# Kernel tuning notes

Hardware: AMD Instinct MI355X
Metric: run time of the kernel (lower is better)

The kernel has to match this reference:

```python
import jax, jax.numpy as jnp
import numpy as np

N = 50000      # nodes
E = 800000     # edges (before self-loops)
H = 8          # attention heads
C = 16         # hidden per head (n_hid)
CH = H * C     # 128 = concat channel width
L = 3          # n_layer
F_IN = 128     # n_feat
N_CLASS = 40
NEG_SLOPE = 0.2


def setup_inputs() -> dict:
    key = jax.random.key(0)
    ks = jax.random.split(key, 14)
    s = 0.1
    return {
        "x": jax.random.normal(ks[0], (N, F_IN), jnp.float32),
        "edge_index": jax.random.randint(ks[1], (2, E), 0, N, jnp.int32),
        # layer 0: in F_IN -> H heads of C
        "W0":   jax.random.normal(ks[2], (F_IN, H * C), jnp.float32) * s,
        "as0":  jax.random.normal(ks[3], (H, C), jnp.float32) * s,
        "ad0":  jax.random.normal(ks[4], (H, C), jnp.float32) * s,
        "b0":   jnp.zeros((H * C,), jnp.float32),
        # layers 1..L-1 (stacked): in CH -> H heads of C
        "W12":  jax.random.normal(ks[5], (L - 1, CH, H * C), jnp.float32) * s,
        "as12": jax.random.normal(ks[6], (L - 1, H, C), jnp.float32) * s,
        "ad12": jax.random.normal(ks[7], (L - 1, H, C), jnp.float32) * s,
        "b12":  jnp.zeros((L - 1, H * C), jnp.float32),
        # attention-based skip aggregation over layers
        "Watt": jax.random.normal(ks[8], (CH, CH), jnp.float32) * s,
        "aatt": jax.random.normal(ks[9], (CH,), jnp.float32) * s,
        # output head
        "Wout": jax.random.normal(ks[10], (CH, N_CLASS), jnp.float32) * s,
        "bout": jnp.zeros((N_CLASS,), jnp.float32),
    }


def _gat_layer(x, W, a_src, a_dst, b, src, dst):
    # x: [N, F]; W: [F, H*C]; a_src/a_dst: [H, C]; b: [H*C]
    h = (x @ W).reshape(N, H, C)                                 # [N,H,C]
    s_src = jnp.einsum("nhc,hc->nh", h, a_src)                   # [N,H]
    s_dst = jnp.einsum("nhc,hc->nh", h, a_dst)                   # [N,H]
    e = jax.nn.leaky_relu(s_src[src] + s_dst[dst], NEG_SLOPE)    # [Et,H]
    # segment softmax over incoming edges of each dst node
    e_max = jax.ops.segment_max(e, dst, num_segments=N)          # [N,H]
    ee = jnp.exp(e - e_max[dst])
    denom = jax.ops.segment_sum(ee, dst, num_segments=N)         # [N,H]
    alpha = ee / (denom[dst] + 1e-16)                            # [Et,H]
    msg = h[src] * alpha[:, :, None]                             # [Et,H,C]
    out = jax.ops.segment_sum(msg, dst, num_segments=N)          # [N,H,C]
    return out.reshape(N, H * C) + b


def reference(x, edge_index, W0, as0, ad0, b0, W12, as12, ad12, b12,
              Watt, aatt, Wout, bout):
    src, dst = edge_index[0], edge_index[1]
    loops = jnp.arange(N, dtype=src.dtype)                       # self-loops (PyG default)
    src = jnp.concatenate([src, loops])
    dst = jnp.concatenate([dst, loops])

    h = jax.nn.elu(_gat_layer(x, W0, as0, ad0, b0, src, dst))
    hs = [h]
    for l in range(L - 1):
        h = jax.nn.elu(_gat_layer(h, W12[l], as12[l], ad12[l], b12[l], src, dst))
        hs.append(h)

    hstack = jnp.stack(hs, axis=1)                               # [N,L,CH]
    scores = jnp.einsum("nlc,c->nl", jnp.tanh(jnp.einsum("nlc,cd->nld", hstack, Watt)), aatt)
    lam = jax.nn.softmax(scores, axis=1)                         # [N,L] over layers
    hfinal = jnp.einsum("nlc,nl->nc", hstack, lam)               # [N,CH]
    return hfinal @ Wout + bout
```

## Files before the change

kernel.cpp:

```cpp
#include <hip/hip_runtime.h>
#include <hip/hip_bf16.h>

typedef float f32x4 __attribute__((ext_vector_type(4)));
typedef short bf16x8 __attribute__((ext_vector_type(8)));

#define BCAP 20480

__device__ __forceinline__ float4 ld4(const float* p){ return *reinterpret_cast<const float4*>(p); }
__device__ __forceinline__ unsigned short f2bf(float f){
  unsigned int u = __float_as_uint(f);
  u = (u + 0x7fffu + ((u>>16)&1u)) >> 16;
  return (unsigned short)u;
}
__device__ __forceinline__ float bflo(unsigned int u){ return __uint_as_float(u<<16); }
__device__ __forceinline__ float bfhi(unsigned int u){ return __uint_as_float(u & 0xffff0000u); }
__device__ __forceinline__ float bfs(short s){ return __uint_as_float(((unsigned)(unsigned short)s)<<16); }
__device__ __forceinline__ float ftanh(float x){
  float e = __expf(2.f*x);
  return fmaf(-2.f, __builtin_amdgcn_rcpf(e+1.f), 1.f);
}

__global__ __launch_bounds__(256) void k_prep_bucket(
    const float* __restrict__ W0, const float* __restrict__ W12, const float* __restrict__ Watt,
    const float* __restrict__ as0, const float* __restrict__ ad0,
    const float* __restrict__ as12, const float* __restrict__ ad12,
    const float* __restrict__ Wout, unsigned short* __restrict__ dst,
    const int* __restrict__ ei, int* __restrict__ bcnt, unsigned* __restrict__ bdata,
    int E_, int Et)
{
  __shared__ char smraw[32768];
  int b = blockIdx.x, t = threadIdx.x;
  if (b < 5){
    if (b == 4){
      unsigned short* wo = dst + (size_t)4*18432;
      for (int i=t; i<48*128; i+=256){
        int col = i>>7, k = i&127;
        float v = (col < 40) ? Wout[(size_t)k*40 + col] : 0.f;
        unsigned short hi = f2bf(v);
        float r = v - __uint_as_float(((unsigned)hi)<<16);
        wo[i] = hi;
        wo[48*128 + i] = f2bf(r);
      }
      return;
    }
    float* Wf = (float*)smraw;
    const float* W = (b==0) ? W0 : (b==3 ? Watt : W12 + (size_t)(b-1)*16384);
    unsigned short* out = dst + (size_t)b*18432;
    const float* as_ = (b==0) ? as0 : as12 + (size_t)(b-1)*128;
    const float* ad_ = (b==0) ? ad0 : ad12 + (size_t)(b-1)*128;

    for (int half=0; half<2; half++){
      #pragma unroll
      for (int p=0;p<8;p++){
        int i = p*256 + t;
        *reinterpret_cast<float4*>(&Wf[i*4]) = ld4(&W[(size_t)half*8192 + i*4]);
      }
      __syncthreads();
      {
        int col = t>>1, koff = (t&1)*32;
        #pragma unroll
        for (int j=0;j<4;j++){
          unsigned short tmp[8];
          #pragma unroll
          for (int q=0;q<8;q++) tmp[q] = f2bf(Wf[(koff + j*8 + q)*128 + col]);
          *reinterpret_cast<uint4*>(&out[col*128 + half*64 + koff + j*8]) = *reinterpret_cast<const uint4*>(tmp);
        }
      }
      {
        int ce = t>>4;
        int h  = ce & 7;
        if (b < 3){
          const float* av = (ce < 8) ? (as_ + h*16) : (ad_ + h*16);
          float avr[16];
          #pragma unroll
          for (int c2=0;c2<16;c2++) avr[c2] = av[c2];
          #pragma unroll
          for (int i=0;i<4;i++){
            int kl = (t&15) + i*16;
            float s = 0.f;
            #pragma unroll
            for (int c2=0;c2<16;c2++) s += Wf[kl*128 + h*16 + c2]*avr[c2];
            out[(128+ce)*128 + half*64 + kl] = f2bf(s);
          }
        } else {
          #pragma unroll
          for (int i=0;i<4;i++){
            int kl = (t&15) + i*16;
            out[(128+ce)*128 + half*64 + kl] = 0;
          }
        }
      }
      __syncthreads();
    }
    return;
  }
  int* h    = (int*)smraw;
  int* base = (int*)(smraw + 256);
  if (t < 64) h[t] = 0;
  __syncthreads();
  int e0 = (b-5)*2048 + t;
  int dv[8], sv[8], rv[8];
  #pragma unroll
  for (int k=0;k<8;k++){
    int e = e0 + k*256;
    if (e < Et){
      int s, d;
      if (e < E_){ s = ei[e]; d = ei[E_+e]; } else { s = e-E_; d = s; }
      dv[k] = d; sv[k] = s;
      rv[k] = atomicAdd(&h[d>>10], 1);
    } else dv[k] = -1;
  }
  __syncthreads();
  if (t < 64 && h[t]) base[t] = atomicAdd(&bcnt[t], h[t]);
  __syncthreads();
  #pragma unroll
  for (int k=0;k<8;k++){
    if (dv[k] >= 0){
      int bk = dv[k]>>10;
      bdata[(size_t)bk*BCAP + base[bk] + rv[k]] = ((unsigned)(dv[k]&1023)<<17) | (unsigned)sv[k];
    }
  }
}

__global__ __launch_bounds__(512) void k_bfinish_gemm0(
    const unsigned* __restrict__ bdata, const int* __restrict__ bcnt,
    int* __restrict__ off, int* __restrict__ csr, int N_, int nb,
    const float* __restrict__ x, const unsigned short* __restrict__ Bt,
    unsigned short* __restrict__ C, float* __restrict__ s_src, float* __restrict__ s_dst)
{
  __shared__ int c[1024];
  __shared__ int wsum[8];
  __shared__ int bbase_s;
  int t = threadIdx.x;
  if ((int)blockIdx.x < nb){
    int b = blockIdx.x;
    if (t < 64){
      int v = (t < nb) ? bcnt[t] : 0;
      int incl = v;
      #pragma unroll
      for (int d=1; d<64; d<<=1){ int u = __shfl_up(incl, d); if (t>=d) incl += u; }
      if (t == b) bbase_s = incl - v;
      if (b == 0 && t == 63) off[N_] = incl;
    }
    int cnt = bcnt[b];
    size_t lo = (size_t)b*BCAP;
    for (int i=t;i<1024;i+=512) c[i]=0;
    __syncthreads();
    for (int i=t; i<cnt; i+=512) atomicAdd(&c[bdata[lo+i]>>17], 1);
    __syncthreads();
    int c0 = c[2*t], c1 = c[2*t+1];
    int s = c0 + c1;
    int lane = t&63, w = t>>6;
    int incl = s;
    #pragma unroll
    for (int d=1; d<64; d<<=1){ int u = __shfl_up(incl, d); if (lane>=d) incl += u; }
    if (lane==63) wsum[w] = incl;
    __syncthreads();
    int wpre = 0;
    #pragma unroll
    for (int k=0;k<8;k++) if (k<w) wpre += wsum[k];
    int run = bbase_s + wpre + incl - s;
    int n = (b<<10) + 2*t;
    if (n   < N_) off[n]   = run;
    if (n+1 < N_) off[n+1] = run + c0;
    c[2*t]   = run;
    c[2*t+1] = run + c0;
    __syncthreads();
    for (int i=t; i<cnt; i+=512){
      unsigned p = bdata[lo+i];
      int pos = atomicAdd(&c[p>>17], 1);
      csr[pos] = (int)(p & 0x1FFFFu);
    }
    return;
  }
  if (t >= 256) return;
  int lane = t & 63, w = t >> 6;
  int rA = lane & 15, g = lane >> 4;
  int r0 = (blockIdx.x - nb)*128 + w*32;
  f32x4 z = {0.f,0.f,0.f,0.f};
  f32x4 acc[2][9];
  #pragma unroll
  for (int mf=0;mf<2;mf++)
    #pragma unroll
    for (int nf=0;nf<9;nf++) acc[mf][nf] = z;

  int M = N_;
  int rowc0 = min(r0 + rA,      M-1);
  int rowc1 = min(r0 + 16 + rA, M-1);
  #pragma unroll
  for (int ks=0; ks<4; ks++){
    int ko = ks*32 + g*8;
    bf16x8 a0, a1;
    float4 v0 = ld4(&x[(size_t)rowc0*128 + ko]);
    float4 v1 = ld4(&x[(size_t)rowc0*128 + ko + 4]);
    float4 v2 = ld4(&x[(size_t)rowc1*128 + ko]);
    float4 v3 = ld4(&x[(size_t)rowc1*128 + ko + 4]);
    a0[0]=(short)f2bf(v0.x); a0[1]=(short)f2bf(v0.y); a0[2]=(short)f2bf(v0.z); a0[3]=(short)f2bf(v0.w);
    a0[4]=(short)f2bf(v1.x); a0[5]=(short)f2bf(v1.y); a0[6]=(short)f2bf(v1.z); a0[7]=(short)f2bf(v1.w);
    a1[0]=(short)f2bf(v2.x); a1[1]=(short)f2bf(v2.y); a1[2]=(short)f2bf(v2.z); a1[3]=(short)f2bf(v2.w);
    a1[4]=(short)f2bf(v3.x); a1[5]=(short)f2bf(v3.y); a1[6]=(short)f2bf(v3.z); a1[7]=(short)f2bf(v3.w);
    #pragma unroll
    for (int nf=0;nf<9;nf++){
      bf16x8 bf_ = *reinterpret_cast<const bf16x8*>(Bt + (size_t)(nf*16+rA)*128 + ko);
      acc[0][nf] = __builtin_amdgcn_mfma_f32_16x16x32_bf16(a0, bf_, acc[0][nf], 0, 0, 0);
      acc[1][nf] = __builtin_amdgcn_mfma_f32_16x16x32_bf16(a1, bf_, acc[1][nf], 0, 0, 0);
    }
  }

  #pragma unroll
  for (int mf=0;mf<2;mf++){
    #pragma unroll
    for (int r=0;r<4;r++){
      int row = r0 + mf*16 + g*4 + r;
      if (row < M){
        #pragma unroll
        for (int nf=0;nf<8;nf++) C[(size_t)row*128 + nf*16 + rA] = f2bf(acc[mf][nf][r]);
        float sv_ = acc[mf][8][r];
        if (rA < 8) s_src[(size_t)row*8 + rA]     = sv_;
        else        s_dst[(size_t)row*8 + rA - 8] = sv_;
      }
    }
  }
}

__global__ __launch_bounds__(256) void k_gemm(
    const unsigned short* __restrict__ A, const unsigned short* __restrict__ Bt,
    unsigned short* __restrict__ C, float* __restrict__ s_src, float* __restrict__ s_dst, int M)
{
  int t = threadIdx.x, lane = t & 63, w = t >> 6;
  int rA = lane & 15, g = lane >> 4;
  int r0 = blockIdx.x*128 + w*32;
  f32x4 z = {0.f,0.f,0.f,0.f};
  f32x4 acc[2][9];
  #pragma unroll
  for (int mf=0;mf<2;mf++)
    #pragma unroll
    for (int nf=0;nf<9;nf++) acc[mf][nf] = z;

  int rowc0 = min(r0 + rA,      M-1);
  int rowc1 = min(r0 + 16 + rA, M-1);
  #pragma unroll
  for (int ks=0; ks<4; ks++){
    int ko = ks*32 + g*8;
    bf16x8 a0 = *reinterpret_cast<const bf16x8*>(A + (size_t)rowc0*128 + ko);
    bf16x8 a1 = *reinterpret_cast<const bf16x8*>(A + (size_t)rowc1*128 + ko);
    #pragma unroll
    for (int nf=0;nf<9;nf++){
      bf16x8 bf_ = *reinterpret_cast<const bf16x8*>(Bt + (size_t)(nf*16+rA)*128 + ko);
      acc[0][nf] = __builtin_amdgcn_mfma_f32_16x16x32_bf16(a0, bf_, acc[0][nf], 0, 0, 0);
      acc[1][nf] = __builtin_amdgcn_mfma_f32_16x16x32_bf16(a1, bf_, acc[1][nf], 0, 0, 0);
    }
  }

  #pragma unroll
  for (int mf=0;mf<2;mf++){
    #pragma unroll
    for (int r=0;r<4;r++){
      int row = r0 + mf*16 + g*4 + r;
      if (row < M){
        #pragma unroll
        for (int nf=0;nf<8;nf++) C[(size_t)row*128 + nf*16 + rA] = f2bf(acc[mf][nf][r]);
        float sv_ = acc[mf][8][r];
        if (rA < 8) s_src[(size_t)row*8 + rA]     = sv_;
        else        s_dst[(size_t)row*8 + rA - 8] = sv_;
      }
    }
  }
}

__global__ __launch_bounds__(256) void k_aggregate(
    const int* __restrict__ off, const int* __restrict__ csr,
    const unsigned short* __restrict__ htmp, const float* __restrict__ s_src,
    const float* __restrict__ s_dst, const float* __restrict__ bias,
    unsigned short* __restrict__ hout, int N_)
{
  __shared__ float esc[4][2][288];
  __shared__ int   ssrc[4][2][32];
  int w = threadIdx.x >> 6;
  int lane = threadIdx.x & 63;
  int half = lane >> 5;
  int l32  = lane & 31;
  int c2   = l32 & 15;
  int eo   = l32 >> 4;
  int myh  = c2 >> 1;
  int n = blockIdx.x*8 + w*2 + half;
  int base = 0, deg = 0;
  if (n < N_){ base = off[n]; deg = off[n+1] - base; }
  float sdv[8] = {0.f,0.f,0.f,0.f,0.f,0.f,0.f,0.f};
  if (n < N_){
    float4 sd0 = ld4(&s_dst[(size_t)n*8]);
    float4 sd1 = ld4(&s_dst[(size_t)n*8+4]);
    sdv[0]=sd0.x; sdv[1]=sd0.y; sdv[2]=sd0.z; sdv[3]=sd0.w;
    sdv[4]=sd1.x; sdv[5]=sd1.y; sdv[6]=sd1.z; sdv[7]=sd1.w;
  }
  float acc0=0.f,acc1=0.f,acc2=0.f,acc3=0.f,acc4=0.f,acc5=0.f,acc6=0.f,acc7=0.f;
  float dsum = 0.f;
  const char* hb = (const char*)htmp + (c2<<4);

  for (int cb=0; cb<deg; cb+=32){
    int cdeg = min(32, deg-cb);
    int srcj = 0;
    float ee[8];
    if (l32 < cdeg){
      srcj = csr[base+cb+l32];
      float4 a0 = ld4(&s_src[(size_t)srcj*8]);
      float4 a1 = ld4(&s_src[(size_t)srcj*8+4]);
      float sv[8] = {a0.x,a0.y,a0.z,a0.w,a1.x,a1.y,a1.z,a1.w};
      #pragma unroll
      for (int h=0;h<8;h++){
        float v = sv[h] + sdv[h];
        v = v > 0.f ? v : 0.2f*v;
        ee[h] = __expf(v);
      }
    } else {
      #pragma unroll
      for (int h=0;h<8;h++) ee[h] = 0.f;
    }
    ssrc[w][half][l32] = srcj;
    #pragma unroll
    for (int h=0;h<8;h++) esc[w][half][h*36 + l32] = ee[h];
    asm volatile("s_waitcnt lgkmcnt(0)" ::: "memory");
    __builtin_amdgcn_sched_barrier(0);

    for (int j=0; j<cdeg; j+=4){
      int e0 = j + eo;
      int e1 = j + 2 + eo;
      int s0 = ssrc[w][half][e0];
      int s1 = ssrc[w][half][e1];
      float ev0 = esc[w][half][myh*36 + e0];
      float ev1 = esc[w][half][myh*36 + e1];
      uint4 u0 = *reinterpret_cast<const uint4*>(hb + ((size_t)(unsigned)s0<<8));
      uint4 u1 = *reinterpret_cast<const uint4*>(hb + ((size_t)(unsigned)s1<<8));
      acc0 = fmaf(ev0, bflo(u0.x), acc0);
      acc1 = fmaf(ev0, bfhi(u0.x), acc1);
      acc2 = fmaf(ev0, bflo(u0.y), acc2);
      acc3 = fmaf(ev0, bfhi(u0.y), acc3);
      acc4 = fmaf(ev0, bflo(u0.z), acc4);
      acc5 = fmaf(ev0, bfhi(u0.z), acc5);
      acc6 = fmaf(ev0, bflo(u0.w), acc6);
      acc7 = fmaf(ev0, bfhi(u0.w), acc7);
      acc0 = fmaf(ev1, bflo(u1.x), acc0);
      acc1 = fmaf(ev1, bfhi(u1.x), acc1);
      acc2 = fmaf(ev1, bflo(u1.y), acc2);
      acc3 = fmaf(ev1, bfhi(u1.y), acc3);
      acc4 = fmaf(ev1, bflo(u1.z), acc4);
      acc5 = fmaf(ev1, bfhi(u1.z), acc5);
      acc6 = fmaf(ev1, bflo(u1.w), acc6);
      acc7 = fmaf(ev1, bfhi(u1.w), acc7);
      dsum += ev0 + ev1;
    }
  }
  acc0 += __shfl_xor(acc0, 16);
  acc1 += __shfl_xor(acc1, 16);
  acc2 += __shfl_xor(acc2, 16);
  acc3 += __shfl_xor(acc3, 16);
  acc4 += __shfl_xor(acc4, 16);
  acc5 += __shfl_xor(acc5, 16);
  acc6 += __shfl_xor(acc6, 16);
  acc7 += __shfl_xor(acc7, 16);
  dsum += __shfl_xor(dsum, 16);

  if (n < N_ && eo == 0){
    float inv = 1.f/(dsum + 1e-16f);
    float4 b0 = ld4(&bias[c2*8]);
    float4 b1 = ld4(&bias[c2*8+4]);
    float o0 = fmaf(acc0, inv, b0.x);
    float o1 = fmaf(acc1, inv, b0.y);
    float o2 = fmaf(acc2, inv, b0.z);
    float o3 = fmaf(acc3, inv, b0.w);
    float o4 = fmaf(acc4, inv, b1.x);
    float o5 = fmaf(acc5, inv, b1.y);
    float o6 = fmaf(acc6, inv, b1.z);
    float o7 = fmaf(acc7, inv, b1.w);
    o0 = o0>0.f ? o0 : (__expf(o0)-1.f);
    o1 = o1>0.f ? o1 : (__expf(o1)-1.f);
    o2 = o2>0.f ? o2 : (__expf(o2)-1.f);
    o3 = o3>0.f ? o3 : (__expf(o3)-1.f);
    o4 = o4>0.f ? o4 : (__expf(o4)-1.f);
    o5 = o5>0.f ? o5 : (__expf(o5)-1.f);
    o6 = o6>0.f ? o6 : (__expf(o6)-1.f);
    o7 = o7>0.f ? o7 : (__expf(o7)-1.f);
    uint4 pk;
    pk.x = (unsigned)f2bf(o0) | ((unsigned)f2bf(o1)<<16);
    pk.y = (unsigned)f2bf(o2) | ((unsigned)f2bf(o3)<<16);
    pk.z = (unsigned)f2bf(o4) | ((unsigned)f2bf(o5)<<16);
    pk.w = (unsigned)f2bf(o6) | ((unsigned)f2bf(o7)<<16);
    *reinterpret_cast<uint4*>(&hout[(size_t)n*128 + c2*8]) = pk;
  }
}

__global__ __launch_bounds__(256) void k_final4(
    const unsigned short* __restrict__ h0, const unsigned short* __restrict__ h1,
    const unsigned short* __restrict__ h2,
    const unsigned short* __restrict__ WattT, const float* __restrict__ aatt,
    const unsigned short* __restrict__ WoutT,
    const float* __restrict__ bout, float* __restrict__ out, int M)
{
  int t = threadIdx.x, lane = t & 63, w = t >> 6;
  int rA = lane & 15, g = lane >> 4;
  int r0 = blockIdx.x*64 + w*16;
  int rowc = min(r0 + rA, M-1);

  float av[8];
  #pragma unroll
  for (int nf=0;nf<8;nf++) av[nf] = aatt[nf*16 + rA];

  bf16x8 a[3][4];
  #pragma unroll
  for (int ks=0;ks<4;ks++){
    int ko = ks*32 + g*8;
    a[0][ks] = *reinterpret_cast<const bf16x8*>(h0 + (size_t)rowc*128 + ko);
    a[1][ks] = *reinterpret_cast<const bf16x8*>(h1 + (size_t)rowc*128 + ko);
    a[2][ks] = *reinterpret_cast<const bf16x8*>(h2 + (size_t)rowc*128 + ko);
  }

  float sc[3][4];
  #pragma unroll
  for (int l=0;l<3;l++)
    #pragma unroll
    for (int r=0;r<4;r++) sc[l][r] = 0.f;

  #pragma unroll
  for (int ch=0; ch<4; ch++){
    f32x4 acc[3][2];
    #pragma unroll
    for (int l=0;l<3;l++){ acc[l][0] = (f32x4){0.f,0.f,0.f,0.f}; acc[l][1] = (f32x4){0.f,0.f,0.f,0.f}; }
    #pragma unroll
    for (int ks=0; ks<4; ks++){
      int ko = ks*32 + g*8;
      bf16x8 b0 = *reinterpret_cast<const bf16x8*>(WattT + (size_t)((ch*2+0)*16+rA)*128 + ko);
      bf16x8 b1 = *reinterpret_cast<const bf16x8*>(WattT + (size_t)((ch*2+1)*16+rA)*128 + ko);
      #pragma unroll
      for (int l=0;l<3;l++){
        acc[l][0] = __builtin_amdgcn_mfma_f32_16x16x32_bf16(a[l][ks], b0, acc[l][0], 0, 0, 0);
        acc[l][1] = __builtin_amdgcn_mfma_f32_16x16x32_bf16(a[l][ks], b1, acc[l][1], 0, 0, 0);
      }
    }
    float w0 = av[ch*2], w1 = av[ch*2+1];
    #pragma unroll
    for (int l=0;l<3;l++)
      #pragma unroll
      for (int r=0;r<4;r++)
        sc[l][r] += ftanh(acc[l][0][r])*w0 + ftanh(acc[l][1][r])*w1;
  }
  #pragma unroll
  for (int l=0;l<3;l++)
    #pragma unroll
    for (int r=0;r<4;r++){
      float s = sc[l][r];
      s += __shfl_xor(s, 1);
      s += __shfl_xor(s, 2);
      s += __shfl_xor(s, 4);
      s += __shfl_xor(s, 8);
      sc[l][r] = s;
    }

  float lam[3][4];
  #pragma unroll
  for (int r=0;r<4;r++){
    float m = fmaxf(sc[0][r], fmaxf(sc[1][r], sc[2][r]));
    float e0 = __expf(sc[0][r]-m), e1 = __expf(sc[1][r]-m), e2 = __expf(sc[2][r]-m);
    float inv = 1.f/(e0+e1+e2);
    lam[0][r]=e0*inv; lam[1][r]=e1*inv; lam[2][r]=e2*inv;
  }
  int rsel = rA & 3;
  int srcLane = ((rA>>2)<<4) | rA;
  float p0 = rsel==0 ? lam[0][0] : rsel==1 ? lam[0][1] : rsel==2 ? lam[0][2] : lam[0][3];
  float p1 = rsel==0 ? lam[1][0] : rsel==1 ? lam[1][1] : rsel==2 ? lam[1][2] : lam[1][3];
  float p2 = rsel==0 ? lam[2][0] : rsel==1 ? lam[2][1] : rsel==2 ? lam[2][2] : lam[2][3];
  float lamA[3];
  lamA[0] = __shfl(p0, srcLane);
  lamA[1] = __shfl(p1, srcLane);
  lamA[2] = __shfl(p2, srcLane);

  f32x4 oacc[3];
  #pragma unroll
  for (int nf=0;nf<3;nf++) oacc[nf] = (f32x4){0.f,0.f,0.f,0.f};
  #pragma unroll
  for (int ks=0;ks<4;ks++){
    int ko = ks*32 + g*8;
    bf16x8 asc[3];
    #pragma unroll
    for (int l=0;l<3;l++){
      #pragma unroll
      for (int i=0;i<8;i++) asc[l][i] = (short)f2bf(bfs(a[l][ks][i]) * lamA[l]);
    }
    #pragma unroll
    for (int nf=0;nf<3;nf++){
      bf16x8 bh = *reinterpret_cast<const bf16x8*>(WoutT + (size_t)(nf*16+rA)*128 + ko);
      bf16x8 bl = *reinterpret_cast<const bf16x8*>(WoutT + 6144 + (size_t)(nf*16+rA)*128 + ko);
      #pragma unroll
      for (int l=0;l<3;l++){
        oacc[nf] = __builtin_amdgcn_mfma_f32_16x16x32_bf16(asc[l], bh, oacc[nf], 0, 0, 0);
        oacc[nf] = __builtin_amdgcn_mfma_f32_16x16x32_bf16(asc[l], bl, oacc[nf], 0, 0, 0);
      }
    }
  }

  #pragma unroll
  for (int nf=0;nf<3;nf++){
    int col = nf*16 + rA;
    float bv = (col < 40) ? bout[col] : 0.f;
    #pragma unroll
    for (int r=0;r<4;r++){
      int row = r0 + g*4 + r;
      if (row < M && col < 40) out[(size_t)row*40 + col] = oacc[nf][r] + bv;
    }
  }
}

extern "C" void kernel_launch(void* const* d_in, const int* in_sizes, int n_in,
                              void* d_out, int out_size, void* d_ws, size_t ws_size,
                              hipStream_t stream)
{
  const float* x    = (const float*)d_in[0];
  const int*   ei   = (const int*)d_in[1];
  const float* W0   = (const float*)d_in[2];
  const float* as0  = (const float*)d_in[3];
  const float* ad0  = (const float*)d_in[4];
  const float* b0   = (const float*)d_in[5];
  const float* W12  = (const float*)d_in[6];
  const float* as12 = (const float*)d_in[7];
  const float* ad12 = (const float*)d_in[8];
  const float* b12  = (const float*)d_in[9];
  const float* Watt = (const float*)d_in[10];
  const float* aatt = (const float*)d_in[11];
  const float* Wout = (const float*)d_in[12];
  const float* bout = (const float*)d_in[13];
  const int N_ = in_sizes[0] / 128;
  const int E_ = in_sizes[1] / 2;
  const int Et = E_ + N_;
  const int nb = (N_ + 1023) >> 10;

  char* p = (char*)d_ws;
  auto carve = [&](size_t bytes)->char*{ char* r = p; p += (bytes + 255) & ~(size_t)255; return r; };
  unsigned short* htmp = (unsigned short*)carve((size_t)N_*128*2);
  unsigned short* h0   = (unsigned short*)carve((size_t)N_*128*2);
  unsigned short* h1   = (unsigned short*)carve((size_t)N_*128*2);
  unsigned short* h2   = (unsigned short*)carve((size_t)N_*128*2);
  unsigned short* wsT  = (unsigned short*)carve((size_t)(5*18432 + 48*128)*2);
  float* ssrc_s  = (float*)carve((size_t)N_*8*4);
  float* sdst_s  = (float*)carve((size_t)N_*8*4);
  int* offv      = (int*)carve((size_t)(N_+1)*4);
  int* bcnt      = (int*)carve((size_t)64*4);
  unsigned* bdata= (unsigned*)carve((size_t)64*BCAP*4);
  int* csr       = (int*)carve((size_t)(Et+8)*4);

  hipMemsetAsync(bcnt, 0, 64*4, stream);
  int gB = (Et + 2047)/2048;
  int gM = (N_+127)/128;
  k_prep_bucket<<<5+gB,256,0,stream>>>(W0, W12, Watt, as0, ad0, as12, ad12, Wout, wsT,
                                       ei, bcnt, bdata, E_, Et);
  k_bfinish_gemm0<<<nb+gM,512,0,stream>>>(bdata, bcnt, offv, csr, N_, nb,
                                          x, wsT, htmp, ssrc_s, sdst_s);

  int gN8 = (N_+7)/8;
  int gF  = (N_+63)/64;
  unsigned short* hl[3] = {h0,h1,h2};
  for (int l=0;l<3;l++){
    const float* bb = (l==0)? b0 : b12 + (size_t)(l-1)*128;
    if (l > 0)
      k_gemm<<<gM,256,0,stream>>>(hl[l-1], wsT + (size_t)l*18432, htmp, ssrc_s, sdst_s, N_);
    k_aggregate<<<gN8,256,0,stream>>>(offv, csr, htmp, ssrc_s, sdst_s, bb, hl[l], N_);
  }
  k_final4<<<gF,256,0,stream>>>(h0, h1, h2, wsT + (size_t)3*18432, aatt,
                                wsT + (size_t)4*18432, bout, (float*)d_out, N_);
}
```

Baseline: 235.0 us.

## Split aggregation channels across two blocks per node group

The GAT aggregation kernel now launches twice as many blocks. Each block handles half of the 128 channels (4 of the 8 heads) for its 8 destination nodes, and within a half-wave each 8-lane group covers 8 edges instead of 16 lanes covering 2 edges. This raises parallelism and halves the softmax score work and LDS per block. In exchange, the CSR indices and source scores are reloaded by both halves, and each gathered row is read in 128-byte halves, giving less contiguous gathers and an extra shuffle-reduction stage.

```diff
diff --git a/kernel.cpp b/kernel.cpp
--- a/kernel.cpp
+++ b/kernel.cpp
@@ -274,61 +274,61 @@
     const float* __restrict__ s_dst, const float* __restrict__ bias,
     unsigned short* __restrict__ hout, int N_)
 {
-  __shared__ float esc[4][2][288];
+  __shared__ float esc[4][2][144];
   __shared__ int   ssrc[4][2][32];
-  int w = threadIdx.x >> 6;
-  int lane = threadIdx.x & 63;
+  int t = threadIdx.x;
+  int w = t >> 6;
+  int lane = t & 63;
   int half = lane >> 5;
   int l32  = lane & 31;
-  int c2   = l32 & 15;
-  int eo   = l32 >> 4;
-  int myh  = c2 >> 1;
-  int n = blockIdx.x*8 + w*2 + half;
+  int c8   = l32 & 7;
+  int eo   = l32 >> 3;
+  int hl   = c8 >> 1;
+  int p    = blockIdx.x & 1;
+  int ng   = blockIdx.x >> 1;
+  int n = ng*8 + w*2 + half;
   int base = 0, deg = 0;
   if (n < N_){ base = off[n]; deg = off[n+1] - base; }
-  float sdv[8] = {0.f,0.f,0.f,0.f,0.f,0.f,0.f,0.f};
+  float sdv[4] = {0.f,0.f,0.f,0.f};
   if (n < N_){
-    float4 sd0 = ld4(&s_dst[(size_t)n*8]);
-    float4 sd1 = ld4(&s_dst[(size_t)n*8+4]);
-    sdv[0]=sd0.x; sdv[1]=sd0.y; sdv[2]=sd0.z; sdv[3]=sd0.w;
-    sdv[4]=sd1.x; sdv[5]=sd1.y; sdv[6]=sd1.z; sdv[7]=sd1.w;
+    float4 sd = ld4(&s_dst[(size_t)n*8 + p*4]);
+    sdv[0]=sd.x; sdv[1]=sd.y; sdv[2]=sd.z; sdv[3]=sd.w;
   }
   float acc0=0.f,acc1=0.f,acc2=0.f,acc3=0.f,acc4=0.f,acc5=0.f,acc6=0.f,acc7=0.f;
   float dsum = 0.f;
-  const char* hb = (const char*)htmp + (c2<<4);
+  const char* hb = (const char*)htmp + (p<<7) + (c8<<4);
 
   for (int cb=0; cb<deg; cb+=32){
     int cdeg = min(32, deg-cb);
     int srcj = 0;
-    float ee[8];
+    float ee[4];
     if (l32 < cdeg){
       srcj = csr[base+cb+l32];
-      float4 a0 = ld4(&s_src[(size_t)srcj*8]);
-      float4 a1 = ld4(&s_src[(size_t)srcj*8+4]);
-      float sv[8] = {a0.x,a0.y,a0.z,a0.w,a1.x,a1.y,a1.z,a1.w};
-      #pragma unroll
-      for (int h=0;h<8;h++){
+      float4 a0 = ld4(&s_src[(size_t)srcj*8 + p*4]);
+      float sv[4] = {a0.x,a0.y,a0.z,a0.w};
+      #pragma unroll
+      for (int h=0;h<4;h++){
         float v = sv[h] + sdv[h];
         v = v > 0.f ? v : 0.2f*v;
         ee[h] = __expf(v);
       }
     } else {
       #pragma unroll
-      for (int h=0;h<8;h++) ee[h] = 0.f;
+      for (int h=0;h<4;h++) ee[h] = 0.f;
     }
     ssrc[w][half][l32] = srcj;
     #pragma unroll
-    for (int h=0;h<8;h++) esc[w][half][h*36 + l32] = ee[h];
+    for (int h=0;h<4;h++) esc[w][half][h*36 + l32] = ee[h];
     asm volatile("s_waitcnt lgkmcnt(0)" ::: "memory");
     __builtin_amdgcn_sched_barrier(0);
 
-    for (int j=0; j<cdeg; j+=4){
+    for (int j=0; j<cdeg; j+=8){
       int e0 = j + eo;
-      int e1 = j + 2 + eo;
+      int e1 = j + 4 + eo;
       int s0 = ssrc[w][half][e0];
       int s1 = ssrc[w][half][e1];
-      float ev0 = esc[w][half][myh*36 + e0];
-      float ev1 = esc[w][half][myh*36 + e1];
+      float ev0 = esc[w][half][hl*36 + e0];
+      float ev1 = esc[w][half][hl*36 + e1];
       uint4 u0 = *reinterpret_cast<const uint4*>(hb + ((size_t)(unsigned)s0<<8));
       uint4 u1 = *reinterpret_cast<const uint4*>(hb + ((size_t)(unsigned)s1<<8));
       acc0 = fmaf(ev0, bflo(u0.x), acc0);
@@ -350,20 +350,21 @@
       dsum += ev0 + ev1;
     }
   }
-  acc0 += __shfl_xor(acc0, 16);
-  acc1 += __shfl_xor(acc1, 16);
-  acc2 += __shfl_xor(acc2, 16);
-  acc3 += __shfl_xor(acc3, 16);
-  acc4 += __shfl_xor(acc4, 16);
-  acc5 += __shfl_xor(acc5, 16);
-  acc6 += __shfl_xor(acc6, 16);
-  acc7 += __shfl_xor(acc7, 16);
-  dsum += __shfl_xor(dsum, 16);
+  acc0 += __shfl_xor(acc0, 8);  acc0 += __shfl_xor(acc0, 16);
+  acc1 += __shfl_xor(acc1, 8);  acc1 += __shfl_xor(acc1, 16);
+  acc2 += __shfl_xor(acc2, 8);  acc2 += __shfl_xor(acc2, 16);
+  acc3 += __shfl_xor(acc3, 8);  acc3 += __shfl_xor(acc3, 16);
+  acc4 += __shfl_xor(acc4, 8);  acc4 += __shfl_xor(acc4, 16);
+  acc5 += __shfl_xor(acc5, 8);  acc5 += __shfl_xor(acc5, 16);
+  acc6 += __shfl_xor(acc6, 8);  acc6 += __shfl_xor(acc6, 16);
+  acc7 += __shfl_xor(acc7, 8);  acc7 += __shfl_xor(acc7, 16);
+  dsum += __shfl_xor(dsum, 8);  dsum += __shfl_xor(dsum, 16);
 
   if (n < N_ && eo == 0){
     float inv = 1.f/(dsum + 1e-16f);
-    float4 b0 = ld4(&bias[c2*8]);
-    float4 b1 = ld4(&bias[c2*8+4]);
+    int cbase = p*64 + c8*8;
+    float4 b0 = ld4(&bias[cbase]);
+    float4 b1 = ld4(&bias[cbase+4]);
     float o0 = fmaf(acc0, inv, b0.x);
     float o1 = fmaf(acc1, inv, b0.y);
     float o2 = fmaf(acc2, inv, b0.z);
@@ -385,7 +386,7 @@
     pk.y = (unsigned)f2bf(o2) | ((unsigned)f2bf(o3)<<16);
     pk.z = (unsigned)f2bf(o4) | ((unsigned)f2bf(o5)<<16);
     pk.w = (unsigned)f2bf(o6) | ((unsigned)f2bf(o7)<<16);
-    *reinterpret_cast<uint4*>(&hout[(size_t)n*128 + c2*8]) = pk;
+    *reinterpret_cast<uint4*>(&hout[(size_t)n*128 + cbase]) = pk;
   }
 }
 
@@ -554,14 +555,14 @@
   k_bfinish_gemm0<<<nb+gM,512,0,stream>>>(bdata, bcnt, offv, csr, N_, nb,
                                           x, wsT, htmp, ssrc_s, sdst_s);
 
-  int gN8 = (N_+7)/8;
+  int gA  = ((N_+7)/8)*2;
   int gF  = (N_+63)/64;
   unsigned short* hl[3] = {h0,h1,h2};
   for (int l=0;l<3;l++){
     const float* bb = (l==0)? b0 : b12 + (size_t)(l-1)*128;
     if (l > 0)
       k_gemm<<<gM,256,0,stream>>>(hl[l-1], wsT + (size_t)l*18432, htmp, ssrc_s, sdst_s, N_);
-    k_aggregate<<<gN8,256,0,stream>>>(offv, csr, htmp, ssrc_s, sdst_s, bb, hl[l], N_);
+    k_aggregate<<<gA,256,0,stream>>>(offv, csr, htmp, ssrc_s, sdst_s, bb, hl[l], N_);
   }
   k_final4<<<gF,256,0,stream>>>(h0, h1, h2, wsT + (size_t)3*18432, aatt,
                                 wsT + (size_t)4*18432, bout, (float*)d_out, N_);
```

After: 238.1 us. About the same (+1.3%).

## Fuse next-layer GEMM into aggregation epilogue with ping-pong buffers

Applied to the files above, without the earlier changes.

Removes the standalone GEMM kernel. After each aggregation block writes its 8 output rows, it also stages them in shared memory and runs the next layer's projection (features plus attention scores) with MFMA. Double-buffered htmp and score arrays keep reads of the current layer's projection separate from writes of the next layer's. This saves two launches and a global re-read of the hidden state. In exchange, each 8-row block reloads the full weight matrix, only half of each MFMA tile holds useful rows, and only two of the four waves do the GEMM work.

```diff
diff --git a/kernel.cpp b/kernel.cpp
--- a/kernel.cpp
+++ b/kernel.cpp
@@ -223,59 +223,18 @@
   }
 }
 
-__global__ __launch_bounds__(256) void k_gemm(
-    const unsigned short* __restrict__ A, const unsigned short* __restrict__ Bt,
-    unsigned short* __restrict__ C, float* __restrict__ s_src, float* __restrict__ s_dst, int M)
-{
-  int t = threadIdx.x, lane = t & 63, w = t >> 6;
-  int rA = lane & 15, g = lane >> 4;
-  int r0 = blockIdx.x*128 + w*32;
-  f32x4 z = {0.f,0.f,0.f,0.f};
-  f32x4 acc[2][9];
-  #pragma unroll
-  for (int mf=0;mf<2;mf++)
-    #pragma unroll
-    for (int nf=0;nf<9;nf++) acc[mf][nf] = z;
-
-  int rowc0 = min(r0 + rA,      M-1);
-  int rowc1 = min(r0 + 16 + rA, M-1);
-  #pragma unroll
-  for (int ks=0; ks<4; ks++){
-    int ko = ks*32 + g*8;
-    bf16x8 a0 = *reinterpret_cast<const bf16x8*>(A + (size_t)rowc0*128 + ko);
-    bf16x8 a1 = *reinterpret_cast<const bf16x8*>(A + (size_t)rowc1*128 + ko);
-    #pragma unroll
-    for (int nf=0;nf<9;nf++){
-      bf16x8 bf_ = *reinterpret_cast<const bf16x8*>(Bt + (size_t)(nf*16+rA)*128 + ko);
-      acc[0][nf] = __builtin_amdgcn_mfma_f32_16x16x32_bf16(a0, bf_, acc[0][nf], 0, 0, 0);
-      acc[1][nf] = __builtin_amdgcn_mfma_f32_16x16x32_bf16(a1, bf_, acc[1][nf], 0, 0, 0);
-    }
-  }
-
-  #pragma unroll
-  for (int mf=0;mf<2;mf++){
-    #pragma unroll
-    for (int r=0;r<4;r++){
-      int row = r0 + mf*16 + g*4 + r;
-      if (row < M){
-        #pragma unroll
-        for (int nf=0;nf<8;nf++) C[(size_t)row*128 + nf*16 + rA] = f2bf(acc[mf][nf][r]);
-        float sv_ = acc[mf][8][r];
-        if (rA < 8) s_src[(size_t)row*8 + rA]     = sv_;
-        else        s_dst[(size_t)row*8 + rA - 8] = sv_;
-      }
-    }
-  }
-}
-
-__global__ __launch_bounds__(256) void k_aggregate(
+template<int FUSE>
+__global__ __launch_bounds__(256) void k_agg_gemm(
     const int* __restrict__ off, const int* __restrict__ csr,
     const unsigned short* __restrict__ htmp, const float* __restrict__ s_src,
     const float* __restrict__ s_dst, const float* __restrict__ bias,
-    unsigned short* __restrict__ hout, int N_)
+    unsigned short* __restrict__ hout, int N_,
+    const unsigned short* __restrict__ Btn,
+    unsigned short* __restrict__ Cn, float* __restrict__ s_srcn, float* __restrict__ s_dstn)
 {
   __shared__ float esc[4][2][288];
   __shared__ int   ssrc[4][2][32];
+  __shared__ unsigned short hrows[8][128];
   int w = threadIdx.x >> 6;
   int lane = threadIdx.x & 63;
   int half = lane >> 5;
@@ -386,6 +345,45 @@
     pk.z = (unsigned)f2bf(o4) | ((unsigned)f2bf(o5)<<16);
     pk.w = (unsigned)f2bf(o6) | ((unsigned)f2bf(o7)<<16);
     *reinterpret_cast<uint4*>(&hout[(size_t)n*128 + c2*8]) = pk;
+    if (FUSE)
+      *reinterpret_cast<uint4*>(&hrows[w*2+half][c2*8]) = pk;
+  }
+
+  if (FUSE){
+    __syncthreads();
+    if (w < 2){
+      int rA2 = lane & 15, g2 = lane >> 4;
+      int rr = rA2 & 7;
+      bf16x8 a2[4];
+      #pragma unroll
+      for (int ks=0;ks<4;ks++)
+        a2[ks] = *reinterpret_cast<const bf16x8*>(&hrows[rr][ks*32 + g2*8]);
+      int n0 = blockIdx.x*8;
+      int nfLo = (w==0) ? 0 : 5;
+      int nfHi = (w==0) ? 5 : 9;
+      for (int nf=nfLo; nf<nfHi; nf++){
+        f32x4 acc2 = {0.f,0.f,0.f,0.f};
+        #pragma unroll
+        for (int ks=0;ks<4;ks++){
+          bf16x8 bf_ = *reinterpret_cast<const bf16x8*>(Btn + (size_t)(nf*16+rA2)*128 + ks*32 + g2*8);
+          acc2 = __builtin_amdgcn_mfma_f32_16x16x32_bf16(a2[ks], bf_, acc2, 0, 0, 0);
+        }
+        if (g2 < 2){
+          #pragma unroll
+          for (int r=0;r<4;r++){
+            int row = g2*4 + r;
+            int n2 = n0 + row;
+            if (n2 < N_){
+              if (nf < 8) Cn[(size_t)n2*128 + nf*16 + rA2] = f2bf(acc2[r]);
+              else {
+                if (rA2 < 8) s_srcn[(size_t)n2*8 + rA2]     = acc2[r];
+                else         s_dstn[(size_t)n2*8 + rA2 - 8] = acc2[r];
+              }
+            }
+          }
+        }
+      }
+    }
   }
 }
 
@@ -534,13 +532,16 @@
 
   char* p = (char*)d_ws;
   auto carve = [&](size_t bytes)->char*{ char* r = p; p += (bytes + 255) & ~(size_t)255; return r; };
-  unsigned short* htmp = (unsigned short*)carve((size_t)N_*128*2);
+  unsigned short* htmpA = (unsigned short*)carve((size_t)N_*128*2);
+  unsigned short* htmpB = (unsigned short*)carve((size_t)N_*128*2);
   unsigned short* h0   = (unsigned short*)carve((size_t)N_*128*2);
   unsigned short* h1   = (unsigned short*)carve((size_t)N_*128*2);
   unsigned short* h2   = (unsigned short*)carve((size_t)N_*128*2);
   unsigned short* wsT  = (unsigned short*)carve((size_t)(5*18432 + 48*128)*2);
-  float* ssrc_s  = (float*)carve((size_t)N_*8*4);
-  float* sdst_s  = (float*)carve((size_t)N_*8*4);
+  float* ssrcA  = (float*)carve((size_t)N_*8*4);
+  float* sdstA  = (float*)carve((size_t)N_*8*4);
+  float* ssrcB  = (float*)carve((size_t)N_*8*4);
+  float* sdstB  = (float*)carve((size_t)N_*8*4);
   int* offv      = (int*)carve((size_t)(N_+1)*4);
   int* bcnt      = (int*)carve((size_t)64*4);
   unsigned* bdata= (unsigned*)carve((size_t)64*BCAP*4);
@@ -552,17 +553,16 @@
   k_prep_bucket<<<5+gB,256,0,stream>>>(W0, W12, Watt, as0, ad0, as12, ad12, Wout, wsT,
                                        ei, bcnt, bdata, E_, Et);
   k_bfinish_gemm0<<<nb+gM,512,0,stream>>>(bdata, bcnt, offv, csr, N_, nb,
-                                          x, wsT, htmp, ssrc_s, sdst_s);
+                                          x, wsT, htmpA, ssrcA, sdstA);
 
   int gN8 = (N_+7)/8;
   int gF  = (N_+63)/64;
-  unsigned short* hl[3] = {h0,h1,h2};
-  for (int l=0;l<3;l++){
-    const float* bb = (l==0)? b0 : b12 + (size_t)(l-1)*128;
-    if (l > 0)
-      k_gemm<<<gM,256,0,stream>>>(hl[l-1], wsT + (size_t)l*18432, htmp, ssrc_s, sdst_s, N_);
-    k_aggregate<<<gN8,256,0,stream>>>(offv, csr, htmp, ssrc_s, sdst_s, bb, hl[l], N_);
-  }
+  k_agg_gemm<1><<<gN8,256,0,stream>>>(offv, csr, htmpA, ssrcA, sdstA, b0, h0, N_,
+                                      wsT + (size_t)1*18432, htmpB, ssrcB, sdstB);
+  k_agg_gemm<1><<<gN8,256,0,stream>>>(offv, csr, htmpB, ssrcB, sdstB, b12, h1, N_,
+                                      wsT + (size_t)2*18432, htmpA, ssrcA, sdstA);
+  k_agg_gemm<0><<<gN8,256,0,stream>>>(offv, csr, htmpA, ssrcA, sdstA, b12 + 128, h2, N_,
+                                      nullptr, nullptr, nullptr, nullptr);
   k_final4<<<gF,256,0,stream>>>(h0, h1, h2, wsT + (size_t)3*18432, aatt,
                                 wsT + (size_t)4*18432, bout, (float*)d_out, N_);
 }
```

Result: faster. 226.9 us (median of 2 runs) (-3.5%).
